# Kernel tuning notes

Measured on AMD Instinct MI355X. Metric: run time of the kernel, lower is better.

## Reference

```python
import jax, jax.numpy as jnp
import numpy as np

B = 256          # number of trees
DEPTH = 8        # complete binary tree depth -> 9 levels
M = 2 ** (DEPTH + 1) - 1   # 511 nodes per tree
N = B * M        # 130816 total nodes
X_SIZE = 128
H_SIZE = 128


def _build_forest():
    j = np.arange(M)
    parent_local = np.maximum((j - 1) // 2, 0)
    lvl = np.array([int(x + 1).bit_length() - 1 for x in j], dtype=np.int32)
    off = (np.arange(B) * M).astype(np.int32)
    parent = (parent_local[None, :] + off[:, None]).reshape(-1).astype(np.int32)
    level = np.tile(lvl, B)
    tree_id = np.repeat(np.arange(B, dtype=np.int32), M)
    isleaf = (level == DEPTH)
    jj = j[1:]
    edge_src = (jj[None, :] + off[:, None]).reshape(-1).astype(np.int32)   # child
    edge_dst = parent[edge_src]                                            # parent
    return parent, level, tree_id, isleaf, edge_src, edge_dst, off


def setup_inputs() -> dict:
    key = jax.random.key(0)
    ks = jax.random.split(key, 12)
    _, level, tree_id, isleaf, edge_src, edge_dst, root_ids = _build_forest()
    sx = 1.0 / np.sqrt(X_SIZE)
    sh = 1.0 / np.sqrt(H_SIZE)
    sxh = 1.0 / np.sqrt(X_SIZE + H_SIZE)
    inp = {
        "X": jax.random.normal(ks[0], (N, X_SIZE), dtype=jnp.float32),
        "h0": jnp.zeros((N, H_SIZE), jnp.float32),
        "c0": jnp.zeros((N, H_SIZE), jnp.float32),
        # bottom-up cell params
        "W_iou_bu": jax.random.normal(ks[1], (3 * H_SIZE, X_SIZE), dtype=jnp.float32) * sx,
        "U_iou_bu": jax.random.normal(ks[2], (3 * H_SIZE, H_SIZE), dtype=jnp.float32) * sh,
        "b_iou_bu": jnp.zeros((1, 3 * H_SIZE), jnp.float32),
        "Uf_bu": jax.random.normal(ks[3], (H_SIZE, H_SIZE), dtype=jnp.float32) * sh,
        "bf_bu": jax.random.normal(ks[4], (H_SIZE,), dtype=jnp.float32) * sh,
        # top-down cell params (x_size = X_SIZE + H_SIZE)
        "W_iou_td": jax.random.normal(ks[5], (3 * H_SIZE, X_SIZE + H_SIZE), dtype=jnp.float32) * sxh,
        "U_iou_td": jax.random.normal(ks[6], (3 * H_SIZE, H_SIZE), dtype=jnp.float32) * sh,
        "b_iou_td": jnp.zeros((1, 3 * H_SIZE), jnp.float32),
        "Uf_td": jax.random.normal(ks[7], (H_SIZE, H_SIZE), dtype=jnp.float32) * sh,
        "bf_td": jax.random.normal(ks[8], (H_SIZE,), dtype=jnp.float32) * sh,
        # graph structure
        "edge_src": jnp.asarray(edge_src),
        "edge_dst": jnp.asarray(edge_dst),
        "level": jnp.asarray(level),
        "tree_id": jnp.asarray(tree_id),
        "isleaf": jnp.asarray(isleaf),
        "root_ids": jnp.asarray(root_ids),
    }
    return inp


def _propagate(X_in, W_iou, U_iou, b_iou, Uf, bf, src, dst, level, no_in, h0, c0, order):
    """Level-synchronous ChildSum TreeLSTM propagation (== dgl.prop_nodes_topo)."""
    n = X_in.shape[0]
    WX = X_in @ W_iou.T                                   # [N, 3H]
    h, c = h0, c0
    for t in order:
        h_src = h[src]                                    # [E, H] gather child/parent states
        c_src = c[src]
        h_tild = jax.ops.segment_sum(h_src, dst, num_segments=n)
        f = jax.nn.sigmoid(h_src @ Uf.T + bf)             # per-edge forget gate
        c_red = jax.ops.segment_sum(f * c_src, dst, num_segments=n)
        iou = WX + h_tild @ U_iou.T + b_iou
        i, o, u = jnp.split(iou, 3, axis=1)
        c_base = jnp.where(no_in[:, None], c0, c_red)     # frontier nodes with no in-edges keep init c
        c_new = jax.nn.sigmoid(i) * jnp.tanh(u) + c_base
        h_new = jax.nn.sigmoid(o) * jnp.tanh(c_new)
        m = (level == t)[:, None]                          # only commit current topological level
        h = jnp.where(m, h_new, h)
        c = jnp.where(m, c_new, c)
    return h


def reference(X, h0, c0, W_iou_bu, U_iou_bu, b_iou_bu, Uf_bu, bf_bu,
              W_iou_td, U_iou_td, b_iou_td, Uf_td, bf_td,
              edge_src, edge_dst, level, tree_id, isleaf, root_ids):
    # bottom-up: messages flow child -> parent, leaves first
    h_bu = _propagate(X, W_iou_bu, U_iou_bu, b_iou_bu, Uf_bu, bf_bu,
                      edge_src, edge_dst, level, isleaf, h0, c0,
                      order=range(DEPTH, -1, -1))
    # top-down: reversed edges, root first
    X_td = jnp.concatenate([X, h_bu], axis=1)
    h_td = _propagate(X_td, W_iou_td, U_iou_td, b_iou_td, Uf_td, bf_td,
                      edge_dst, edge_src, level, level == 0, h0, c0,
                      order=range(0, DEPTH + 1))
    root_h_bottom_up = h_bu[root_ids]                     # [B, H]
    leaf = isleaf.astype(h_td.dtype)
    sums = jax.ops.segment_sum(h_td * leaf[:, None], tree_id, num_segments=root_ids.shape[0])
    cnt = jax.ops.segment_sum(leaf, tree_id, num_segments=root_ids.shape[0])
    leaves_h_top_down = sums / cnt[:, None]               # per-tree mean over leaves
    return jnp.concatenate([root_h_bottom_up, leaves_h_top_down], axis=1)
```

## Files before the change

kernel.cpp:

```cpp
#include <hip/hip_runtime.h>
#include <cmath>

#define NTREE 256
#define MPT 511
#define NNODE (NTREE * MPT)
#define HS 128

typedef __bf16 bf16x8 __attribute__((ext_vector_type(8)));
typedef float  f32x4  __attribute__((ext_vector_type(4)));

__device__ __forceinline__ float sigf(float x) {
  float e = __builtin_amdgcn_exp2f(x * -1.44269504f);
  return __builtin_amdgcn_rcpf(1.0f + e);
}
__device__ __forceinline__ float tanh_fast(float x) {
  float e = __builtin_amdgcn_exp2f(x * -2.88539008f);
  return __builtin_amdgcn_rcpf(1.0f + e) * 2.0f - 1.0f;
}
__device__ __forceinline__ f32x4 mm(bf16x8 a, bf16x8 b, f32x4 c) {
  return __builtin_amdgcn_mfma_f32_16x16x32_bf16(a, b, c, 0, 0, 0);
}
__device__ __forceinline__ int swz(int row, int rb, int kb) { return row * rb + (kb ^ ((row & 7) << 4)); }
__device__ __forceinline__ void st8(char* s, int row, int rb, int chunk, bf16x8 v) {
  *reinterpret_cast<bf16x8*>(s + swz(row, rb, chunk * 16)) = v;
}
__device__ __forceinline__ bf16x8 ld8(const char* s, int row, int rb, int kb) {
  return *reinterpret_cast<const bf16x8*>(s + swz(row, rb, kb));
}
__device__ __forceinline__ bf16x8 g8(const __bf16* p) { return *reinterpret_cast<const bf16x8*>(p); }
__device__ __forceinline__ bf16x8 gx8(const float* p) {
  float4 v0 = reinterpret_cast<const float4*>(p)[0];
  float4 v1 = reinterpret_cast<const float4*>(p)[1];
  bf16x8 o;
  o[0] = (__bf16)v0.x; o[1] = (__bf16)v0.y; o[2] = (__bf16)v0.z; o[3] = (__bf16)v0.w;
  o[4] = (__bf16)v1.x; o[5] = (__bf16)v1.y; o[6] = (__bf16)v1.z; o[7] = (__bf16)v1.w;
  return o;
}
__device__ __forceinline__ void stbf(char* s, int row, int rb, int kbyte, float v) {
  *reinterpret_cast<__bf16*>(s + row * rb + (kbyte ^ ((row & 7) << 4))) = (__bf16)v;
}

__global__ void __launch_bounds__(512, 1)
bu_bottom(const float* __restrict__ Xf,
          const __bf16* __restrict__ W, const float* __restrict__ bp,
          const __bf16* __restrict__ Uf, const float* __restrict__ bf_,
          __bf16* __restrict__ h_bu, float* __restrict__ cws)
{
  __shared__ __align__(16) char sX8[64 * 256];
  __shared__ __align__(16) char sX7[32 * 256];
  __shared__ __align__(16) char sT [32 * 256];
  __shared__ float sCr[32][128];

  const int tid = threadIdx.x, w = tid >> 6, l = tid & 63, lr = l & 15, lk = l >> 4;
  const int ch = w * 16 + lr;
  const int vb = blockIdx.x * 32;
  const int b  = vb >> 7;
  const int j7 = 127 + (vb & 127);
  const size_t g7  = (size_t)b * MPT + j7;
  const size_t gLf = (size_t)b * MPT + 2 * j7 + 1;
  const size_t gp6 = (size_t)b * MPT + ((j7 - 1) >> 1);

  bf16x8 Wb[8][3], Uff[4];
#pragma unroll
  for (int ks = 0; ks < 8; ++ks)
#pragma unroll
    for (int g2 = 0; g2 < 3; ++g2)
      Wb[ks][g2] = g8(W + (size_t)(g2 * 128 + ch) * 256 + ks * 32 + lk * 8);
#pragma unroll
  for (int ks = 0; ks < 4; ++ks) Uff[ks] = g8(Uf + (size_t)ch * HS + ks * 32 + lk * 8);

#pragma unroll
  for (int it = 0; it < 2; ++it) {
    int idx = tid + it * 512, n = idx >> 4, e = idx & 15;
    st8(sX8, n, 256, e, gx8(Xf + (gLf + n) * HS + e * 8));
  }
  { int n = tid >> 4, e = tid & 15;
    st8(sX7, n, 256, e, gx8(Xf + (g7 + n) * HS + e * 8)); }

  const float bia = bp[ch], boa = bp[ch + 128], bua = bp[ch + 256], bfa = bf_[ch];
  __syncthreads();

  f32x4 acc[3][4];
#pragma unroll
  for (int g2 = 0; g2 < 3; ++g2)
#pragma unroll
    for (int mf = 0; mf < 4; ++mf) acc[g2][mf] = 0.0f;

#pragma unroll
  for (int ks = 0; ks < 4; ++ks) {
    const int kb = ks * 64 + lk * 16;
    bf16x8 A0 = ld8(sX8, lr,      256, kb);
    bf16x8 A1 = ld8(sX8, 16 + lr, 256, kb);
    bf16x8 A2 = ld8(sX8, 32 + lr, 256, kb);
    bf16x8 A3 = ld8(sX8, 48 + lr, 256, kb);
#pragma unroll
    for (int g2 = 0; g2 < 3; ++g2) {
      acc[g2][0] = mm(A0, Wb[ks][g2], acc[g2][0]);
      acc[g2][1] = mm(A1, Wb[ks][g2], acc[g2][1]);
      acc[g2][2] = mm(A2, Wb[ks][g2], acc[g2][2]);
      acc[g2][3] = mm(A3, Wb[ks][g2], acc[g2][3]);
    }
  }
  float cnv[4][4], hnv[4][4];
#pragma unroll
  for (int mf = 0; mf < 4; ++mf)
#pragma unroll
    for (int j = 0; j < 4; ++j) {
      const int nrow = 16 * mf + lk * 4 + j;
      float cn = sigf(acc[0][mf][j] + bia) * tanh_fast(acc[2][mf][j] + bua);
      float hn = sigf(acc[1][mf][j] + boa) * tanh_fast(cn);
      cnv[mf][j] = cn; hnv[mf][j] = hn;
      h_bu[(gLf + nrow) * HS + ch] = (__bf16)hn;
    }
  __syncthreads();
#pragma unroll
  for (int mf = 0; mf < 4; ++mf)
#pragma unroll
    for (int j = 0; j < 4; ++j)
      stbf(sX8, 16 * mf + lk * 4 + j, 256, 2 * ch, hnv[mf][j]);
  __syncthreads();
  {
    f32x4 fa[4];
#pragma unroll
    for (int mf = 0; mf < 4; ++mf) fa[mf] = 0.0f;
#pragma unroll
    for (int ks = 0; ks < 4; ++ks) {
      const int kb = ks * 64 + lk * 16;
      fa[0] = mm(ld8(sX8, lr,      256, kb), Uff[ks], fa[0]);
      fa[1] = mm(ld8(sX8, 16 + lr, 256, kb), Uff[ks], fa[1]);
      fa[2] = mm(ld8(sX8, 32 + lr, 256, kb), Uff[ks], fa[2]);
      fa[3] = mm(ld8(sX8, 48 + lr, 256, kb), Uff[ks], fa[3]);
    }
#pragma unroll
    for (int mf = 0; mf < 4; ++mf)
#pragma unroll
      for (int p = 0; p < 2; ++p) {
        const int er = 16 * mf + lk * 4 + 2 * p;
        const int pr = er >> 1;
        float f0 = sigf(fa[mf][2 * p]     + bfa) * cnv[mf][2 * p];
        float f1 = sigf(fa[mf][2 * p + 1] + bfa) * cnv[mf][2 * p + 1];
        sCr[pr][ch] = f0 + f1;
        stbf(sT, pr, 256, 2 * ch, hnv[mf][2 * p] + hnv[mf][2 * p + 1]);
      }
  }
  __syncthreads();

  f32x4 ac2[3][2];
#pragma unroll
  for (int g2 = 0; g2 < 3; ++g2) { ac2[g2][0] = 0.0f; ac2[g2][1] = 0.0f; }
#pragma unroll
  for (int ks = 0; ks < 8; ++ks) {
    const int kb = (ks & 3) * 64 + lk * 16;
    bf16x8 A0 = (ks < 4) ? ld8(sX7, lr,      256, kb) : ld8(sT, lr,      256, kb);
    bf16x8 A1 = (ks < 4) ? ld8(sX7, 16 + lr, 256, kb) : ld8(sT, 16 + lr, 256, kb);
#pragma unroll
    for (int g2 = 0; g2 < 3; ++g2) {
      ac2[g2][0] = mm(A0, Wb[ks][g2], ac2[g2][0]);
      ac2[g2][1] = mm(A1, Wb[ks][g2], ac2[g2][1]);
    }
  }
  float cn2[2][4], hn2[2][4];
#pragma unroll
  for (int mf = 0; mf < 2; ++mf)
#pragma unroll
    for (int j = 0; j < 4; ++j) {
      const int nr = 16 * mf + lk * 4 + j;
      float cn = sigf(ac2[0][mf][j] + bia) * tanh_fast(ac2[2][mf][j] + bua) + sCr[nr][ch];
      float hn = sigf(ac2[1][mf][j] + boa) * tanh_fast(cn);
      cn2[mf][j] = cn; hn2[mf][j] = hn;
      h_bu[(g7 + nr) * HS + ch] = (__bf16)hn;
    }
  __syncthreads();
#pragma unroll
  for (int mf = 0; mf < 2; ++mf)
#pragma unroll
    for (int j = 0; j < 4; ++j)
      stbf(sX7, 16 * mf + lk * 4 + j, 256, 2 * ch, hn2[mf][j]);
  __syncthreads();
  {
    f32x4 fb[2]; fb[0] = 0.0f; fb[1] = 0.0f;
#pragma unroll
    for (int ks = 0; ks < 4; ++ks) {
      const int kb = ks * 64 + lk * 16;
      fb[0] = mm(ld8(sX7, lr,      256, kb), Uff[ks], fb[0]);
      fb[1] = mm(ld8(sX7, 16 + lr, 256, kb), Uff[ks], fb[1]);
    }
#pragma unroll
    for (int mf = 0; mf < 2; ++mf)
#pragma unroll
      for (int p = 0; p < 2; ++p) {
        const int er = 16 * mf + lk * 4 + 2 * p;
        const size_t gp = gp6 + (er >> 1);
        float f0 = sigf(fb[mf][2 * p]     + bfa) * cn2[mf][2 * p];
        float f1 = sigf(fb[mf][2 * p + 1] + bfa) * cn2[mf][2 * p + 1];
        cws[gp * HS + ch] = f0 + f1;
        h_bu[gp * HS + ch] = (__bf16)(hn2[mf][2 * p] + hn2[mf][2 * p + 1]);
      }
  }
}

__global__ void __launch_bounds__(512, 1)
td_bottom(const float* __restrict__ Xf,
          const __bf16* __restrict__ W, const float* __restrict__ bp,
          const __bf16* __restrict__ Uf, const float* __restrict__ bf_,
          const __bf16* __restrict__ h_bu, const __bf16* __restrict__ h_td,
          const float* __restrict__ cws, float* __restrict__ part)
{
  __shared__ __align__(16) char sA7[32 * 768];
  __shared__ __align__(16) char sXH[64 * 512];
  __shared__ __align__(16) char sTd[32 * 256];
  __shared__ float sFc[32][128];

  const int tid = threadIdx.x, w = tid >> 6, l = tid & 63, lr = l & 15, lk = l >> 4;
  const int ch = w * 16 + lr;
  const int vb = blockIdx.x * 32;
  const int b  = vb >> 7;
  const int j7 = 127 + (vb & 127);
  const size_t g7  = (size_t)b * MPT + j7;
  const size_t gLf = (size_t)b * MPT + 2 * j7 + 1;
  const size_t gp6 = (size_t)b * MPT + ((j7 - 1) >> 1);

  bf16x8 Wt[12][3], Uff[4];
#pragma unroll
  for (int ks = 0; ks < 12; ++ks)
#pragma unroll
    for (int g2 = 0; g2 < 3; ++g2)
      Wt[ks][g2] = g8(W + (size_t)(g2 * 128 + ch) * 384 + ks * 32 + lk * 8);
#pragma unroll
  for (int ks = 0; ks < 4; ++ks) Uff[ks] = g8(Uf + (size_t)ch * HS + ks * 32 + lk * 8);

  { int n = tid >> 4, e = tid & 15;
    st8(sA7, n, 768, e,      gx8(Xf   + (g7 + n) * HS + e * 8));
    st8(sA7, n, 768, 16 + e, g8(h_bu + (g7 + n) * HS + e * 8));
    st8(sA7, n, 768, 32 + e, g8(h_td + (gp6 + (n >> 1)) * HS + e * 8)); }
#pragma unroll
  for (int it = 0; it < 2; ++it) {
    int idx = tid + it * 512, n = idx >> 4, e = idx & 15;
    st8(sXH, n, 512, e,      gx8(Xf   + (gLf + n) * HS + e * 8));
    st8(sXH, n, 512, 16 + e, g8(h_bu + (gLf + n) * HS + e * 8));
  }
  float cb[2][4];
#pragma unroll
  for (int mf = 0; mf < 2; ++mf)
#pragma unroll
    for (int j = 0; j < 4; ++j) {
      const int nr = 16 * mf + lk * 4 + j;
      cb[mf][j] = cws[(gp6 + (nr >> 1)) * HS + ch];
    }
  const float bia = bp[ch], boa = bp[ch + 128], bua = bp[ch + 256], bfa = bf_[ch];
  __syncthreads();

  f32x4 ac[3][2];
#pragma unroll
  for (int g2 = 0; g2 < 3; ++g2) { ac[g2][0] = 0.0f; ac[g2][1] = 0.0f; }
#pragma unroll
  for (int ks = 0; ks < 12; ++ks) {
    const int kb = ks * 64 + lk * 16;
    bf16x8 A0 = ld8(sA7, lr,      768, kb);
    bf16x8 A1 = ld8(sA7, 16 + lr, 768, kb);
#pragma unroll
    for (int g2 = 0; g2 < 3; ++g2) {
      ac[g2][0] = mm(A0, Wt[ks][g2], ac[g2][0]);
      ac[g2][1] = mm(A1, Wt[ks][g2], ac[g2][1]);
    }
  }
  float cn7[2][4];
#pragma unroll
  for (int mf = 0; mf < 2; ++mf)
#pragma unroll
    for (int j = 0; j < 4; ++j) {
      const int nr = 16 * mf + lk * 4 + j;
      float cn = sigf(ac[0][mf][j] + bia) * tanh_fast(ac[2][mf][j] + bua) + cb[mf][j];
      float hn = sigf(ac[1][mf][j] + boa) * tanh_fast(cn);
      cn7[mf][j] = cn;
      stbf(sTd, nr, 256, 2 * ch, hn);
    }
  __syncthreads();
  {
    f32x4 fa[2]; fa[0] = 0.0f; fa[1] = 0.0f;
#pragma unroll
    for (int ks = 0; ks < 4; ++ks) {
      const int kb = ks * 64 + lk * 16;
      fa[0] = mm(ld8(sTd, lr,      256, kb), Uff[ks], fa[0]);
      fa[1] = mm(ld8(sTd, 16 + lr, 256, kb), Uff[ks], fa[1]);
    }
#pragma unroll
    for (int mf = 0; mf < 2; ++mf)
#pragma unroll
      for (int j = 0; j < 4; ++j) {
        const int nr = 16 * mf + lk * 4 + j;
        sFc[nr][ch] = sigf(fa[mf][j] + bfa) * cn7[mf][j];
      }
  }
  __syncthreads();

  f32x4 a8[3][4];
#pragma unroll
  for (int g2 = 0; g2 < 3; ++g2)
#pragma unroll
    for (int mf = 0; mf < 4; ++mf) a8[g2][mf] = 0.0f;
#pragma unroll
  for (int ks = 0; ks < 12; ++ks) {
    bf16x8 A0, A1, A2, A3;
    if (ks < 8) {
      const int kb = ks * 64 + lk * 16;
      A0 = ld8(sXH, lr,      512, kb);
      A1 = ld8(sXH, 16 + lr, 512, kb);
      A2 = ld8(sXH, 32 + lr, 512, kb);
      A3 = ld8(sXH, 48 + lr, 512, kb);
    } else {
      const int kb = (ks - 8) * 64 + lk * 16;
      A0 = ld8(sTd, (lr >> 1),      256, kb);
      A1 = ld8(sTd, 8 + (lr >> 1),  256, kb);
      A2 = ld8(sTd, 16 + (lr >> 1), 256, kb);
      A3 = ld8(sTd, 24 + (lr >> 1), 256, kb);
    }
#pragma unroll
    for (int g2 = 0; g2 < 3; ++g2) {
      a8[g2][0] = mm(A0, Wt[ks][g2], a8[g2][0]);
      a8[g2][1] = mm(A1, Wt[ks][g2], a8[g2][1]);
      a8[g2][2] = mm(A2, Wt[ks][g2], a8[g2][2]);
      a8[g2][3] = mm(A3, Wt[ks][g2], a8[g2][3]);
    }
  }
  float psum = 0.0f;
#pragma unroll
  for (int mf = 0; mf < 4; ++mf)
#pragma unroll
    for (int j = 0; j < 4; ++j) {
      const int nrow = 16 * mf + lk * 4 + j;
      float cbase = sFc[nrow >> 1][ch];
      float cn = sigf(a8[0][mf][j] + bia) * tanh_fast(a8[2][mf][j] + bua) + cbase;
      float hn = sigf(a8[1][mf][j] + boa) * tanh_fast(cn);
      psum += hn;
    }
  float s = psum;
  s += __shfl_xor(s, 16);
  s += __shfl_xor(s, 32);
  if (lk == 0) part[(size_t)blockIdx.x * 128 + ch] = s;
}

template <int MODE>
__global__ void __launch_bounds__(256, 2)
level_big(int t,
          const float*  __restrict__ Xf,
          const __bf16* __restrict__ W,
          const float*  __restrict__ bp,
          const __bf16* __restrict__ Uf,
          const float*  __restrict__ bf_,
          __bf16* __restrict__ h_bu,
          __bf16* __restrict__ h_td,
          float*  __restrict__ cws)
{
  constexpr int KA = (MODE == 1) ? 256 : 384;
  constexpr int KS = KA / 32;
  constexpr int BK = (MODE == 3) ? 384 : 256;
  constexpr int RB = KA * 2;
  constexpr int HB = (MODE == 1) ? 256 : 512;

  __shared__ __align__(16) char sA[64 * RB];
  __shared__ int sG[64], sP[64];

  const int tid = threadIdx.x;
  const int w = tid >> 6, l = tid & 63, lr = l & 15, lk = l >> 4;

  if (tid < 64) {
    int v = blockIdx.x * 64 + tid;
    int b = v >> t;
    int j = (1 << t) - 1 + (v & ((1 << t) - 1));
    sG[tid] = b * MPT + j;
    sP[tid] = b * MPT + ((j - 1) >> 1);
  }
  __syncthreads();

#pragma unroll
  for (int it = 0; it < 4; ++it) {
    int idx = tid + it * 256, n = idx >> 4, e = idx & 15;
    st8(sA, n, RB, e, gx8(Xf + (size_t)sG[n] * HS + e * 8));
  }
#pragma unroll
  for (int it = 0; it < 4; ++it) {
    int idx = tid + it * 256, n = idx >> 4, e = idx & 15;
    st8(sA, n, RB, 16 + e, g8(h_bu + (size_t)sG[n] * HS + e * 8));
  }
  if constexpr (MODE == 3) {
#pragma unroll
    for (int it = 0; it < 4; ++it) {
      int idx = tid + it * 256, n = idx >> 4, e = idx & 15;
      st8(sA, n, RB, 32 + e, g8(h_td + (size_t)sP[n] * HS + e * 8));
    }
  }
  __syncthreads();

  float cb[2][4][4];
  float bia[2], boa[2], bua[2], bfa[2];
#pragma unroll
  for (int nf = 0; nf < 2; ++nf) {
    const int ch = w * 32 + nf * 16 + lr;
    bia[nf] = bp[ch]; boa[nf] = bp[ch + 128]; bua[nf] = bp[ch + 256];
    bfa[nf] = bf_[ch];
#pragma unroll
    for (int mf = 0; mf < 4; ++mf)
#pragma unroll
      for (int j = 0; j < 4; ++j) {
        const int nrow = 16 * mf + lk * 4 + j;
        const int src = (MODE == 1) ? sG[nrow] : sP[nrow];
        cb[nf][mf][j] = cws[(size_t)src * HS + ch];
      }
  }

  f32x4 acc[6][4];
#pragma unroll
  for (int p = 0; p < 6; ++p)
#pragma unroll
    for (int mf = 0; mf < 4; ++mf) acc[p][mf] = 0.0f;

  bf16x8 A0[4], A1[4], Bb[3][6];
  auto ldA = [&](int ks, bf16x8* Ad) {
#pragma unroll
    for (int mf = 0; mf < 4; ++mf) Ad[mf] = ld8(sA, mf * 16 + lr, RB, ks * 64 + lk * 16);
  };
  auto ldB = [&](int ks, int s) {
#pragma unroll
    for (int g2 = 0; g2 < 3; ++g2)
#pragma unroll
      for (int nf = 0; nf < 2; ++nf)
        Bb[s][g2 * 2 + nf] = g8(W + (size_t)(g2 * 128 + w * 32 + nf * 16 + lr) * BK + ks * 32 + lk * 8);
  };

  ldB(0, 0); ldA(0, A0); ldB(1, 1);
#pragma unroll
  for (int ks = 0; ks < KS; ++ks) {
    bf16x8* Ac = (ks & 1) ? A1 : A0;
    bf16x8* An = (ks & 1) ? A0 : A1;
    if (ks + 1 < KS) ldA(ks + 1, An);
    if (ks + 2 < KS) ldB(ks + 2, (ks + 2) % 3);
#pragma unroll
    for (int p = 0; p < 6; ++p)
#pragma unroll
      for (int mf = 0; mf < 4; ++mf) acc[p][mf] = mm(Ac[mf], Bb[ks % 3][p], acc[p][mf]);
  }

  bf16x8 Uff[8];
#pragma unroll
  for (int ks = 0; ks < 4; ++ks)
#pragma unroll
    for (int nf = 0; nf < 2; ++nf)
      Uff[ks * 2 + nf] = g8(Uf + (size_t)(w * 32 + nf * 16 + lr) * HS + ks * 32 + lk * 8);

  __bf16* hp = (MODE == 3) ? h_td : h_bu;
  float cnv[2][4][4], hnv[2][4][4];
#pragma unroll
  for (int nf = 0; nf < 2; ++nf) {
    const int ch = w * 32 + nf * 16 + lr;
#pragma unroll
    for (int mf = 0; mf < 4; ++mf)
#pragma unroll
      for (int j = 0; j < 4; ++j) {
        const int nrow = 16 * mf + lk * 4 + j;
        float cn = sigf(acc[nf][mf][j] + bia[nf]) * tanh_fast(acc[4 + nf][mf][j] + bua[nf]) + cb[nf][mf][j];
        float hn = sigf(acc[2 + nf][mf][j] + boa[nf]) * tanh_fast(cn);
        hp[(size_t)sG[nrow] * HS + ch] = (__bf16)hn;
        cnv[nf][mf][j] = cn; hnv[nf][mf][j] = hn;
      }
  }

  __syncthreads();
#pragma unroll
  for (int nf = 0; nf < 2; ++nf) {
    const int ch = w * 32 + nf * 16 + lr;
#pragma unroll
    for (int mf = 0; mf < 4; ++mf)
#pragma unroll
      for (int j = 0; j < 4; ++j)
        stbf(sA, 16 * mf + lk * 4 + j, RB, HB + 2 * ch, hnv[nf][mf][j]);
  }
  __syncthreads();
  f32x4 fa[4][2];
#pragma unroll
  for (int mf = 0; mf < 4; ++mf) { fa[mf][0] = 0.0f; fa[mf][1] = 0.0f; }
#pragma unroll
  for (int ks = 0; ks < 4; ++ks) {
    bf16x8 a0 = ld8(sA, lr,      RB, HB + ks * 64 + lk * 16);
    bf16x8 a1 = ld8(sA, 16 + lr, RB, HB + ks * 64 + lk * 16);
    bf16x8 a2 = ld8(sA, 32 + lr, RB, HB + ks * 64 + lk * 16);
    bf16x8 a3 = ld8(sA, 48 + lr, RB, HB + ks * 64 + lk * 16);
#pragma unroll
    for (int nf = 0; nf < 2; ++nf) {
      fa[0][nf] = mm(a0, Uff[ks * 2 + nf], fa[0][nf]);
      fa[1][nf] = mm(a1, Uff[ks * 2 + nf], fa[1][nf]);
      fa[2][nf] = mm(a2, Uff[ks * 2 + nf], fa[2][nf]);
      fa[3][nf] = mm(a3, Uff[ks * 2 + nf], fa[3][nf]);
    }
  }
#pragma unroll
  for (int nf = 0; nf < 2; ++nf) {
    const int ch = w * 32 + nf * 16 + lr;
    if constexpr (MODE == 3) {
#pragma unroll
      for (int mf = 0; mf < 4; ++mf)
#pragma unroll
        for (int j = 0; j < 4; ++j) {
          const int nrow = 16 * mf + lk * 4 + j;
          cws[(size_t)sG[nrow] * HS + ch] = sigf(fa[mf][nf][j] + bfa[nf]) * cnv[nf][mf][j];
        }
    } else {
#pragma unroll
      for (int mf = 0; mf < 4; ++mf)
#pragma unroll
        for (int p = 0; p < 2; ++p) {
          const int er = 16 * mf + lk * 4 + 2 * p;
          float f0 = sigf(fa[mf][nf][2 * p]     + bfa[nf]) * cnv[nf][mf][2 * p];
          float f1 = sigf(fa[mf][nf][2 * p + 1] + bfa[nf]) * cnv[nf][mf][2 * p + 1];
          const int gp = sP[er];
          cws[(size_t)gp * HS + ch] = f0 + f1;
          h_bu[(size_t)gp * HS + ch] = (__bf16)(hnv[nf][mf][2 * p] + hnv[nf][mf][2 * p + 1]);
        }
    }
  }
}

__global__ void __launch_bounds__(512, 2)
small_both(const float* __restrict__ Xf,
           const __bf16* __restrict__ Wbu, const float* __restrict__ bbu,
           const __bf16* __restrict__ Ufb, const float* __restrict__ bfb,
           const __bf16* __restrict__ Wtd, const float* __restrict__ btd,
           const __bf16* __restrict__ Uft, const float* __restrict__ bft,
           __bf16* __restrict__ h_bu, __bf16* __restrict__ h_td,
           float* __restrict__ cws)
{
  __shared__ __align__(16) char sX[31 * 256];
  __shared__ __align__(16) char sH[31 * 256];
  __shared__ __align__(16) char sT[16 * 256];
  __shared__ __align__(16) char sTd[15 * 256];
  __shared__ float sCr[16][128];
  __shared__ float sFc[16][128];

  const int tid = threadIdx.x, w = tid >> 6, l = tid & 63, lr = l & 15, lk = l >> 4;
  const int ch = w * 16 + lr;
  const size_t base = (size_t)blockIdx.x * MPT * HS;

  for (int idx = tid; idx < 31 * 16; idx += 512) {
    int n = idx >> 4, e = idx & 15;
    st8(sX, n, 256, e, gx8(Xf + base + (size_t)n * HS + e * 8));
  }
  if (tid < 256) { int n = tid >> 4, e = tid & 15;
    st8(sT, n, 256, e, g8(h_bu + base + (size_t)(15 + n) * HS + e * 8)); }
  { int n = tid >> 5, e = tid & 31;
    reinterpret_cast<float4*>(&sCr[n][0])[e] =
        reinterpret_cast<const float4*>(cws + base + (size_t)(15 + n) * HS)[e]; }
  for (int idx = tid; idx < 15 * 16; idx += 512)
    *reinterpret_cast<float4*>(sTd + idx * 16) = float4{0.f, 0.f, 0.f, 0.f};

  {
    const float bia = bbu[ch], boa = bbu[ch + 128], bua = bbu[ch + 256], bfa = bfb[ch];
    bf16x8 Wb[8][3], Uff[4];
#pragma unroll
    for (int ks = 0; ks < 8; ++ks)
#pragma unroll
      for (int g2 = 0; g2 < 3; ++g2)
        Wb[ks][g2] = g8(Wbu + (size_t)(g2 * 128 + ch) * 256 + ks * 32 + lk * 8);
#pragma unroll
    for (int ks = 0; ks < 4; ++ks)
      Uff[ks] = g8(Ufb + (size_t)ch * HS + ks * 32 + lk * 8);
    __syncthreads();

    for (int t = 4; t >= 0; --t) {
      const int cnt = 1 << t, j0 = cnt - 1;
      f32x4 acc0 = 0.0f, acc1 = 0.0f, acc2 = 0.0f;
      bf16x8 Aa[3];
      auto ldA = [&](int ks, int s) {
        const int kb = (ks & 3) * 64 + lk * 16;
        Aa[s] = (ks < 4) ? ld8(sX, j0 + lr, 256, kb) : ld8(sT, lr, 256, kb);
      };
      ldA(0, 0); ldA(1, 1);
#pragma unroll
      for (int ks = 0; ks < 8; ++ks) {
        if (ks + 2 < 8) ldA(ks + 2, (ks + 2) % 3);
        acc0 = mm(Aa[ks % 3], Wb[ks][0], acc0);
        acc1 = mm(Aa[ks % 3], Wb[ks][1], acc1);
        acc2 = mm(Aa[ks % 3], Wb[ks][2], acc2);
      }
      float cnv[4], hnv[4];
#pragma unroll
      for (int j = 0; j < 4; ++j) {
        const int r = lk * 4 + j;
        float cn = sigf(acc0[j] + bia) * tanh_fast(acc2[j] + bua) + sCr[r][ch];
        float hn = sigf(acc1[j] + boa) * tanh_fast(cn);
        cnv[j] = cn; hnv[j] = hn;
        if (r < cnt) stbf(sH, j0 + r, 256, 2 * ch, hn);
      }
      if (t == 0 && lk == 0) h_bu[base + ch] = (__bf16)hnv[0];
      __syncthreads();
      if (t > 0) {
        f32x4 fa = 0.0f;
#pragma unroll
        for (int ks = 0; ks < 4; ++ks)
          fa = mm(ld8(sH, j0 + lr, 256, ks * 64 + lk * 16), Uff[ks], fa);
#pragma unroll
        for (int p = 0; p < 2; ++p) {
          const int pr = lk * 2 + p;
          if (pr < (cnt >> 1)) {
            float f0 = sigf(fa[2 * p]     + bfa) * cnv[2 * p];
            float f1 = sigf(fa[2 * p + 1] + bfa) * cnv[2 * p + 1];
            sCr[pr][ch] = f0 + f1;
            stbf(sT, pr, 256, 2 * ch, hnv[2 * p] + hnv[2 * p + 1]);
          }
        }
      }
      __syncthreads();
    }
  }

  {
    const float bia = btd[ch], boa = btd[ch + 128], bua = btd[ch + 256], bfa = bft[ch];
    bf16x8 Wt[12][3], Uff[4];
#pragma unroll
    for (int ks = 0; ks < 12; ++ks)
#pragma unroll
      for (int g2 = 0; g2 < 3; ++g2)
        Wt[ks][g2] = g8(Wtd + (size_t)(g2 * 128 + ch) * 384 + ks * 32 + lk * 8);
#pragma unroll
    for (int ks = 0; ks < 4; ++ks)
      Uff[ks] = g8(Uft + (size_t)ch * HS + ks * 32 + lk * 8);

    for (int t = 0; t <= 4; ++t) {
      const int cnt = 1 << t, j0 = cnt - 1;
      f32x4 acc0 = 0.0f, acc1 = 0.0f, acc2 = 0.0f;
      bf16x8 Aa[3];
      auto ldA = [&](int ks, int s) {
        const int kb = (ks & 3) * 64 + lk * 16;
        if (ks < 4)      Aa[s] = ld8(sX, j0 + lr, 256, kb);
        else if (ks < 8) Aa[s] = ld8(sH, j0 + lr, 256, kb);
        else { int pr = (j0 + lr - 1) >> 1; pr = pr < 0 ? 0 : pr;
               Aa[s] = ld8(sTd, pr, 256, kb); }
      };
      ldA(0, 0); ldA(1, 1);
#pragma unroll
      for (int ks = 0; ks < 12; ++ks) {
        if (ks + 2 < 12) ldA(ks + 2, (ks + 2) % 3);
        acc0 = mm(Aa[ks % 3], Wt[ks][0], acc0);
        acc1 = mm(Aa[ks % 3], Wt[ks][1], acc1);
        acc2 = mm(Aa[ks % 3], Wt[ks][2], acc2);
      }
      float cnv[4], hnv[4];
#pragma unroll
      for (int j = 0; j < 4; ++j) {
        const int r = lk * 4 + j;
        float cbv = (t == 0) ? 0.0f : sFc[r >> 1][ch];
        float cn = sigf(acc0[j] + bia) * tanh_fast(acc2[j] + bua) + cbv;
        float hn = sigf(acc1[j] + boa) * tanh_fast(cn);
        cnv[j] = cn; hnv[j] = hn;
        stbf(sT, r, 256, 2 * ch, hn);
        if (r < cnt && j0 + r < 15) stbf(sTd, j0 + r, 256, 2 * ch, hn);
        if (t == 4) h_td[base + (size_t)(15 + r) * HS + ch] = (__bf16)hn;
      }
      __syncthreads();
      f32x4 fa = 0.0f;
#pragma unroll
      for (int ks = 0; ks < 4; ++ks)
        fa = mm(ld8(sT, lr, 256, ks * 64 + lk * 16), Uff[ks], fa);
#pragma unroll
      for (int j = 0; j < 4; ++j) {
        const int r = lk * 4 + j;
        float fcv = sigf(fa[j] + bfa) * cnv[j];
        if (r < cnt) {
          if (t < 4) sFc[r][ch] = fcv;
          else       cws[base + (size_t)(15 + r) * HS + ch] = fcv;
        }
      }
      __syncthreads();
    }
  }
}

__global__ void __launch_bounds__(256)
prep(const float* __restrict__ Wbu, const float* __restrict__ Ubu,
     const float* __restrict__ Wtd, const float* __restrict__ Utd,
     const float* __restrict__ Ufb, const float* __restrict__ Uft,
     __bf16* wbu, __bf16* wtd, __bf16* ufb, __bf16* uft)
{
  int i = blockIdx.x * 256 + threadIdx.x;
  if (i < 98304) {
    int r = i >> 8, c = i & 255;
    wbu[i] = (__bf16)(c < 128 ? Wbu[r * 128 + c] : Ubu[r * 128 + c - 128]);
  } else if (i < 245760) {
    int k = i - 98304; int r = k / 384, c = k - r * 384;
    wtd[k] = (__bf16)(c < 256 ? Wtd[r * 256 + c] : Utd[r * 128 + (c - 256)]);
  } else if (i < 262144) {
    int k = i - 245760; ufb[k] = (__bf16)Ufb[k];
  } else {
    int k = i - 262144; uft[k] = (__bf16)Uft[k];
  }
}

__global__ void __launch_bounds__(128)
finalize_kernel(const __bf16* __restrict__ h_bu, const float* __restrict__ part,
                float* __restrict__ out)
{
  int b = blockIdx.x, ch = threadIdx.x;
  out[(size_t)b * 256 + ch] = (float)h_bu[((size_t)b * MPT) * HS + ch];
  const float* pp = part + (size_t)b * 512 + ch;
  out[(size_t)b * 256 + 128 + ch] = (pp[0] + pp[128] + pp[256] + pp[384]) * (1.0f / 256.0f);
}

extern "C" void kernel_launch(void* const* d_in, const int* in_sizes, int n_in,
                              void* d_out, int out_size, void* d_ws, size_t ws_size,
                              hipStream_t stream) {
  const float* X     = (const float*)d_in[0];
  const float* W_bu  = (const float*)d_in[3];
  const float* U_bu  = (const float*)d_in[4];
  const float* b_bu  = (const float*)d_in[5];
  const float* Uf_bu = (const float*)d_in[6];
  const float* bf_bu = (const float*)d_in[7];
  const float* W_td  = (const float*)d_in[8];
  const float* U_td  = (const float*)d_in[9];
  const float* b_td  = (const float*)d_in[10];
  const float* Uf_td = (const float*)d_in[11];
  const float* bf_td = (const float*)d_in[12];

  char* p = (char*)d_ws;
  __bf16* wbu  = (__bf16*)p; p += (size_t)384 * 256 * 2;
  __bf16* wtd  = (__bf16*)p; p += (size_t)384 * 384 * 2;
  __bf16* ufb  = (__bf16*)p; p += (size_t)128 * 128 * 2;
  __bf16* uft  = (__bf16*)p; p += (size_t)128 * 128 * 2;
  __bf16* h_bu = (__bf16*)p; p += (size_t)NNODE * HS * 2;
  __bf16* h_td = (__bf16*)p; p += (size_t)NNODE * HS * 2;
  float*  cws  = (float*)p;  p += (size_t)NNODE * HS * 4;
  float*  part = (float*)p;

  prep<<<1088, 256, 0, stream>>>(W_bu, U_bu, W_td, U_td, Uf_bu, Uf_td, wbu, wtd, ufb, uft);

  bu_bottom<<<1024, 512, 0, stream>>>(X, wbu, b_bu, ufb, bf_bu, h_bu, cws);
  level_big<1><<<256, 256, 0, stream>>>(6, X, wbu, b_bu, ufb, bf_bu, h_bu, h_td, cws);
  level_big<1><<<128, 256, 0, stream>>>(5, X, wbu, b_bu, ufb, bf_bu, h_bu, h_td, cws);

  small_both<<<256, 512, 0, stream>>>(X, wbu, b_bu, ufb, bf_bu,
                                      wtd, b_td, uft, bf_td, h_bu, h_td, cws);

  level_big<3><<<128, 256, 0, stream>>>(5, X, wtd, b_td, uft, bf_td, h_bu, h_td, cws);
  level_big<3><<<256, 256, 0, stream>>>(6, X, wtd, b_td, uft, bf_td, h_bu, h_td, cws);
  td_bottom<<<1024, 512, 0, stream>>>(X, wtd, b_td, uft, bf_td, h_bu, h_td, cws, part);

  finalize_kernel<<<256, 128, 0, stream>>>(h_bu, part, (float*)d_out);
}
```

Measured before the change: 237.2 us.

## Double per-block node tile in bottom-level BU/TD kernels to amortize weight loads

bu_bottom and td_bottom now handle 64 level-7 nodes (128 leaves) per block instead of 32, halving the grid to 512 blocks. Each block loads the full register-resident weight fragments once, so the total weight traffic and setup per node is halved. td_bottom also stages the parent h_td rows once in a separate compact buffer instead of duplicating them per child row. The cost is doubled LDS use and larger accumulator arrays, which raise register pressure and risk spills, and the grid now gives about two blocks per CU.

Measured after the change: 291.0 us. +22.7%, slower.

```diff
diff --git a/kernel.cpp b/kernel.cpp
--- a/kernel.cpp
+++ b/kernel.cpp
@@ -46,14 +46,14 @@
           const __bf16* __restrict__ Uf, const float* __restrict__ bf_,
           __bf16* __restrict__ h_bu, float* __restrict__ cws)
 {
-  __shared__ __align__(16) char sX8[64 * 256];
-  __shared__ __align__(16) char sX7[32 * 256];
-  __shared__ __align__(16) char sT [32 * 256];
-  __shared__ float sCr[32][128];
+  __shared__ __align__(16) char sX8[128 * 256];
+  __shared__ __align__(16) char sX7[64 * 256];
+  __shared__ __align__(16) char sT [64 * 256];
+  __shared__ float sCr[64][128];
 
   const int tid = threadIdx.x, w = tid >> 6, l = tid & 63, lr = l & 15, lk = l >> 4;
   const int ch = w * 16 + lr;
-  const int vb = blockIdx.x * 32;
+  const int vb = blockIdx.x * 64;
   const int b  = vb >> 7;
   const int j7 = 127 + (vb & 127);
   const size_t g7  = (size_t)b * MPT + j7;
@@ -70,131 +70,135 @@
   for (int ks = 0; ks < 4; ++ks) Uff[ks] = g8(Uf + (size_t)ch * HS + ks * 32 + lk * 8);
 
 #pragma unroll
+  for (int it = 0; it < 4; ++it) {
+    int idx = tid + it * 512, n = idx >> 4, e = idx & 15;
+    st8(sX8, n, 256, e, gx8(Xf + (gLf + n) * HS + e * 8));
+  }
+#pragma unroll
   for (int it = 0; it < 2; ++it) {
     int idx = tid + it * 512, n = idx >> 4, e = idx & 15;
-    st8(sX8, n, 256, e, gx8(Xf + (gLf + n) * HS + e * 8));
-  }
-  { int n = tid >> 4, e = tid & 15;
-    st8(sX7, n, 256, e, gx8(Xf + (g7 + n) * HS + e * 8)); }
+    st8(sX7, n, 256, e, gx8(Xf + (g7 + n) * HS + e * 8));
+  }
 
   const float bia = bp[ch], boa = bp[ch + 128], bua = bp[ch + 256], bfa = bf_[ch];
   __syncthreads();
 
-  f32x4 acc[3][4];
+  f32x4 acc[3][8];
 #pragma unroll
   for (int g2 = 0; g2 < 3; ++g2)
 #pragma unroll
-    for (int mf = 0; mf < 4; ++mf) acc[g2][mf] = 0.0f;
+    for (int q = 0; q < 8; ++q) acc[g2][q] = 0.0f;
 
 #pragma unroll
   for (int ks = 0; ks < 4; ++ks) {
     const int kb = ks * 64 + lk * 16;
-    bf16x8 A0 = ld8(sX8, lr,      256, kb);
-    bf16x8 A1 = ld8(sX8, 16 + lr, 256, kb);
-    bf16x8 A2 = ld8(sX8, 32 + lr, 256, kb);
-    bf16x8 A3 = ld8(sX8, 48 + lr, 256, kb);
-#pragma unroll
-    for (int g2 = 0; g2 < 3; ++g2) {
-      acc[g2][0] = mm(A0, Wb[ks][g2], acc[g2][0]);
-      acc[g2][1] = mm(A1, Wb[ks][g2], acc[g2][1]);
-      acc[g2][2] = mm(A2, Wb[ks][g2], acc[g2][2]);
-      acc[g2][3] = mm(A3, Wb[ks][g2], acc[g2][3]);
-    }
-  }
-  float cnv[4][4], hnv[4][4];
-#pragma unroll
-  for (int mf = 0; mf < 4; ++mf)
+    bf16x8 Aq[8];
+#pragma unroll
+    for (int q = 0; q < 8; ++q) Aq[q] = ld8(sX8, 16 * q + lr, 256, kb);
+#pragma unroll
+    for (int g2 = 0; g2 < 3; ++g2)
+#pragma unroll
+      for (int q = 0; q < 8; ++q) acc[g2][q] = mm(Aq[q], Wb[ks][g2], acc[g2][q]);
+  }
+  float cnv[8][4], hnv[8][4];
+#pragma unroll
+  for (int q = 0; q < 8; ++q)
 #pragma unroll
     for (int j = 0; j < 4; ++j) {
-      const int nrow = 16 * mf + lk * 4 + j;
-      float cn = sigf(acc[0][mf][j] + bia) * tanh_fast(acc[2][mf][j] + bua);
-      float hn = sigf(acc[1][mf][j] + boa) * tanh_fast(cn);
-      cnv[mf][j] = cn; hnv[mf][j] = hn;
+      const int nrow = 16 * q + lk * 4 + j;
+      float cn = sigf(acc[0][q][j] + bia) * tanh_fast(acc[2][q][j] + bua);
+      float hn = sigf(acc[1][q][j] + boa) * tanh_fast(cn);
+      cnv[q][j] = cn; hnv[q][j] = hn;
       h_bu[(gLf + nrow) * HS + ch] = (__bf16)hn;
     }
   __syncthreads();
 #pragma unroll
-  for (int mf = 0; mf < 4; ++mf)
+  for (int q = 0; q < 8; ++q)
 #pragma unroll
     for (int j = 0; j < 4; ++j)
-      stbf(sX8, 16 * mf + lk * 4 + j, 256, 2 * ch, hnv[mf][j]);
+      stbf(sX8, 16 * q + lk * 4 + j, 256, 2 * ch, hnv[q][j]);
   __syncthreads();
   {
-    f32x4 fa[4];
-#pragma unroll
-    for (int mf = 0; mf < 4; ++mf) fa[mf] = 0.0f;
+    f32x4 fa[8];
+#pragma unroll
+    for (int q = 0; q < 8; ++q) fa[q] = 0.0f;
 #pragma unroll
     for (int ks = 0; ks < 4; ++ks) {
       const int kb = ks * 64 + lk * 16;
-      fa[0] = mm(ld8(sX8, lr,      256, kb), Uff[ks], fa[0]);
-      fa[1] = mm(ld8(sX8, 16 + lr, 256, kb), Uff[ks], fa[1]);
-      fa[2] = mm(ld8(sX8, 32 + lr, 256, kb), Uff[ks], fa[2]);
-      fa[3] = mm(ld8(sX8, 48 + lr, 256, kb), Uff[ks], fa[3]);
-    }
-#pragma unroll
-    for (int mf = 0; mf < 4; ++mf)
+#pragma unroll
+      for (int q = 0; q < 8; ++q)
+        fa[q] = mm(ld8(sX8, 16 * q + lr, 256, kb), Uff[ks], fa[q]);
+    }
+#pragma unroll
+    for (int q = 0; q < 8; ++q)
 #pragma unroll
       for (int p = 0; p < 2; ++p) {
-        const int er = 16 * mf + lk * 4 + 2 * p;
+        const int er = 16 * q + lk * 4 + 2 * p;
         const int pr = er >> 1;
-        float f0 = sigf(fa[mf][2 * p]     + bfa) * cnv[mf][2 * p];
-        float f1 = sigf(fa[mf][2 * p + 1] + bfa) * cnv[mf][2 * p + 1];
+        float f0 = sigf(fa[q][2 * p]     + bfa) * cnv[q][2 * p];
+        float f1 = sigf(fa[q][2 * p + 1] + bfa) * cnv[q][2 * p + 1];
         sCr[pr][ch] = f0 + f1;
-        stbf(sT, pr, 256, 2 * ch, hnv[mf][2 * p] + hnv[mf][2 * p + 1]);
-      }
-  }
-  __syncthreads();
-
-  f32x4 ac2[3][2];
-#pragma unroll
-  for (int g2 = 0; g2 < 3; ++g2) { ac2[g2][0] = 0.0f; ac2[g2][1] = 0.0f; }
+        stbf(sT, pr, 256, 2 * ch, hnv[q][2 * p] + hnv[q][2 * p + 1]);
+      }
+  }
+  __syncthreads();
+
+  f32x4 ac2[3][4];
+#pragma unroll
+  for (int g2 = 0; g2 < 3; ++g2)
+#pragma unroll
+    for (int q = 0; q < 4; ++q) ac2[g2][q] = 0.0f;
 #pragma unroll
   for (int ks = 0; ks < 8; ++ks) {
     const int kb = (ks & 3) * 64 + lk * 16;
-    bf16x8 A0 = (ks < 4) ? ld8(sX7, lr,      256, kb) : ld8(sT, lr,      256, kb);
-    bf16x8 A1 = (ks < 4) ? ld8(sX7, 16 + lr, 256, kb) : ld8(sT, 16 + lr, 256, kb);
-#pragma unroll
-    for (int g2 = 0; g2 < 3; ++g2) {
-      ac2[g2][0] = mm(A0, Wb[ks][g2], ac2[g2][0]);
-      ac2[g2][1] = mm(A1, Wb[ks][g2], ac2[g2][1]);
-    }
-  }
-  float cn2[2][4], hn2[2][4];
-#pragma unroll
-  for (int mf = 0; mf < 2; ++mf)
+    bf16x8 Aq[4];
+#pragma unroll
+    for (int q = 0; q < 4; ++q)
+      Aq[q] = (ks < 4) ? ld8(sX7, 16 * q + lr, 256, kb) : ld8(sT, 16 * q + lr, 256, kb);
+#pragma unroll
+    for (int g2 = 0; g2 < 3; ++g2)
+#pragma unroll
+      for (int q = 0; q < 4; ++q) ac2[g2][q] = mm(Aq[q], Wb[ks][g2], ac2[g2][q]);
+  }
+  float cn2[4][4], hn2[4][4];
+#pragma unroll
+  for (int q = 0; q < 4; ++q)
 #pragma unroll
     for (int j = 0; j < 4; ++j) {
-      const int nr = 16 * mf + lk * 4 + j;
-      float cn = sigf(ac2[0][mf][j] + bia) * tanh_fast(ac2[2][mf][j] + bua) + sCr[nr][ch];
-      float hn = sigf(ac2[1][mf][j] + boa) * tanh_fast(cn);
-      cn2[mf][j] = cn; hn2[mf][j] = hn;
+      const int nr = 16 * q + lk * 4 + j;
+      float cn = sigf(ac2[0][q][j] + bia) * tanh_fast(ac2[2][q][j] + bua) + sCr[nr][ch];
+      float hn = sigf(ac2[1][q][j] + boa) * tanh_fast(cn);
+      cn2[q][j] = cn; hn2[q][j] = hn;
       h_bu[(g7 + nr) * HS + ch] = (__bf16)hn;
     }
   __syncthreads();
 #pragma unroll
-  for (int mf = 0; mf < 2; ++mf)
+  for (int q = 0; q < 4; ++q)
 #pragma unroll
     for (int j = 0; j < 4; ++j)
-      stbf(sX7, 16 * mf + lk * 4 + j, 256, 2 * ch, hn2[mf][j]);
+      stbf(sX7, 16 * q + lk * 4 + j, 256, 2 * ch, hn2[q][j]);
   __syncthreads();
   {
-    f32x4 fb[2]; fb[0] = 0.0f; fb[1] = 0.0f;
+    f32x4 fb[4];
+#pragma unroll
+    for (int q = 0; q < 4; ++q) fb[q] = 0.0f;
 #pragma unroll
     for (int ks = 0; ks < 4; ++ks) {
       const int kb = ks * 64 + lk * 16;
-      fb[0] = mm(ld8(sX7, lr,      256, kb), Uff[ks], fb[0]);
-      fb[1] = mm(ld8(sX7, 16 + lr, 256, kb), Uff[ks], fb[1]);
-    }
-#pragma unroll
-    for (int mf = 0; mf < 2; ++mf)
+#pragma unroll
+      for (int q = 0; q < 4; ++q)
+        fb[q] = mm(ld8(sX7, 16 * q + lr, 256, kb), Uff[ks], fb[q]);
+    }
+#pragma unroll
+    for (int q = 0; q < 4; ++q)
 #pragma unroll
       for (int p = 0; p < 2; ++p) {
-        const int er = 16 * mf + lk * 4 + 2 * p;
+        const int er = 16 * q + lk * 4 + 2 * p;
         const size_t gp = gp6 + (er >> 1);
-        float f0 = sigf(fb[mf][2 * p]     + bfa) * cn2[mf][2 * p];
-        float f1 = sigf(fb[mf][2 * p + 1] + bfa) * cn2[mf][2 * p + 1];
+        float f0 = sigf(fb[q][2 * p]     + bfa) * cn2[q][2 * p];
+        float f1 = sigf(fb[q][2 * p + 1] + bfa) * cn2[q][2 * p + 1];
         cws[gp * HS + ch] = f0 + f1;
-        h_bu[gp * HS + ch] = (__bf16)(hn2[mf][2 * p] + hn2[mf][2 * p + 1]);
+        h_bu[gp * HS + ch] = (__bf16)(hn2[q][2 * p] + hn2[q][2 * p + 1]);
       }
   }
 }
@@ -206,14 +210,15 @@
           const __bf16* __restrict__ h_bu, const __bf16* __restrict__ h_td,
           const float* __restrict__ cws, float* __restrict__ part)
 {
-  __shared__ __align__(16) char sA7[32 * 768];
-  __shared__ __align__(16) char sXH[64 * 512];
-  __shared__ __align__(16) char sTd[32 * 256];
-  __shared__ float sFc[32][128];
+  __shared__ __align__(16) char sA7[64 * 512];
+  __shared__ __align__(16) char sPar[32 * 256];
+  __shared__ __align__(16) char sXH[128 * 512];
+  __shared__ __align__(16) char sTd[64 * 256];
+  __shared__ float sFc[64][128];
 
   const int tid = threadIdx.x, w = tid >> 6, l = tid & 63, lr = l & 15, lk = l >> 4;
   const int ch = w * 16 + lr;
-  const int vb = blockIdx.x * 32;
+  const int vb = blockIdx.x * 64;
   const int b  = vb >> 7;
   const int j7 = 127 + (vb & 127);
   const size_t g7  = (size_t)b * MPT + j7;
@@ -229,109 +234,118 @@
 #pragma unroll
   for (int ks = 0; ks < 4; ++ks) Uff[ks] = g8(Uf + (size_t)ch * HS + ks * 32 + lk * 8);
 
+#pragma unroll
+  for (int it = 0; it < 2; ++it) {
+    int idx = tid + it * 512, n = idx >> 4, e = idx & 15;
+    st8(sA7, n, 512, e,      gx8(Xf   + (g7 + n) * HS + e * 8));
+    st8(sA7, n, 512, 16 + e, g8(h_bu + (g7 + n) * HS + e * 8));
+  }
   { int n = tid >> 4, e = tid & 15;
-    st8(sA7, n, 768, e,      gx8(Xf   + (g7 + n) * HS + e * 8));
-    st8(sA7, n, 768, 16 + e, g8(h_bu + (g7 + n) * HS + e * 8));
-    st8(sA7, n, 768, 32 + e, g8(h_td + (gp6 + (n >> 1)) * HS + e * 8)); }
-#pragma unroll
-  for (int it = 0; it < 2; ++it) {
+    if (tid < 512) st8(sPar, n & 31, 256, e,
+                       g8(h_td + (gp6 + (n & 31)) * HS + e * 8)); }
+#pragma unroll
+  for (int it = 0; it < 4; ++it) {
     int idx = tid + it * 512, n = idx >> 4, e = idx & 15;
     st8(sXH, n, 512, e,      gx8(Xf   + (gLf + n) * HS + e * 8));
     st8(sXH, n, 512, 16 + e, g8(h_bu + (gLf + n) * HS + e * 8));
   }
-  float cb[2][4];
-#pragma unroll
-  for (int mf = 0; mf < 2; ++mf)
+  float cb[4][4];
+#pragma unroll
+  for (int q = 0; q < 4; ++q)
 #pragma unroll
     for (int j = 0; j < 4; ++j) {
-      const int nr = 16 * mf + lk * 4 + j;
-      cb[mf][j] = cws[(gp6 + (nr >> 1)) * HS + ch];
+      const int nr = 16 * q + lk * 4 + j;
+      cb[q][j] = cws[(gp6 + (nr >> 1)) * HS + ch];
     }
   const float bia = bp[ch], boa = bp[ch + 128], bua = bp[ch + 256], bfa = bf_[ch];
   __syncthreads();
 
-  f32x4 ac[3][2];
-#pragma unroll
-  for (int g2 = 0; g2 < 3; ++g2) { ac[g2][0] = 0.0f; ac[g2][1] = 0.0f; }
+  f32x4 ac[3][4];
+#pragma unroll
+  for (int g2 = 0; g2 < 3; ++g2)
+#pragma unroll
+    for (int q = 0; q < 4; ++q) ac[g2][q] = 0.0f;
 #pragma unroll
   for (int ks = 0; ks < 12; ++ks) {
-    const int kb = ks * 64 + lk * 16;
-    bf16x8 A0 = ld8(sA7, lr,      768, kb);
-    bf16x8 A1 = ld8(sA7, 16 + lr, 768, kb);
-#pragma unroll
-    for (int g2 = 0; g2 < 3; ++g2) {
-      ac[g2][0] = mm(A0, Wt[ks][g2], ac[g2][0]);
-      ac[g2][1] = mm(A1, Wt[ks][g2], ac[g2][1]);
-    }
-  }
-  float cn7[2][4];
-#pragma unroll
-  for (int mf = 0; mf < 2; ++mf)
+    bf16x8 Aq[4];
+    if (ks < 8) {
+      const int kb = ks * 64 + lk * 16;
+#pragma unroll
+      for (int q = 0; q < 4; ++q) Aq[q] = ld8(sA7, 16 * q + lr, 512, kb);
+    } else {
+      const int kb = (ks - 8) * 64 + lk * 16;
+#pragma unroll
+      for (int q = 0; q < 4; ++q) Aq[q] = ld8(sPar, 8 * q + (lr >> 1), 256, kb);
+    }
+#pragma unroll
+    for (int g2 = 0; g2 < 3; ++g2)
+#pragma unroll
+      for (int q = 0; q < 4; ++q) ac[g2][q] = mm(Aq[q], Wt[ks][g2], ac[g2][q]);
+  }
+  float cn7[4][4];
+#pragma unroll
+  for (int q = 0; q < 4; ++q)
 #pragma unroll
     for (int j = 0; j < 4; ++j) {
-      const int nr = 16 * mf + lk * 4 + j;
-      float cn = sigf(ac[0][mf][j] + bia) * tanh_fast(ac[2][mf][j] + bua) + cb[mf][j];
-      float hn = sigf(ac[1][mf][j] + boa) * tanh_fast(cn);
-      cn7[mf][j] = cn;
+      const int nr = 16 * q + lk * 4 + j;
+      float cn = sigf(ac[0][q][j] + bia) * tanh_fast(ac[2][q][j] + bua) + cb[q][j];
+      float hn = sigf(ac[1][q][j] + boa) * tanh_fast(cn);
+      cn7[q][j] = cn;
       stbf(sTd, nr, 256, 2 * ch, hn);
     }
   __syncthreads();
   {
-    f32x4 fa[2]; fa[0] = 0.0f; fa[1] = 0.0f;
+    f32x4 fa[4];
+#pragma unroll
+    for (int q = 0; q < 4; ++q) fa[q] = 0.0f;
 #pragma unroll
     for (int ks = 0; ks < 4; ++ks) {
       const int kb = ks * 64 + lk * 16;
-      fa[0] = mm(ld8(sTd, lr,      256, kb), Uff[ks], fa[0]);
-      fa[1] = mm(ld8(sTd, 16 + lr, 256, kb), Uff[ks], fa[1]);
-    }
-#pragma unroll
-    for (int mf = 0; mf < 2; ++mf)
+#pragma unroll
+      for (int q = 0; q < 4; ++q)
+        fa[q] = mm(ld8(sTd, 16 * q + lr, 256, kb), Uff[ks], fa[q]);
+    }
+#pragma unroll
+    for (int q = 0; q < 4; ++q)
 #pragma unroll
       for (int j = 0; j < 4; ++j) {
-        const int nr = 16 * mf + lk * 4 + j;
-        sFc[nr][ch] = sigf(fa[mf][j] + bfa) * cn7[mf][j];
-      }
-  }
-  __syncthreads();
-
-  f32x4 a8[3][4];
+        const int nr = 16 * q + lk * 4 + j;
+        sFc[nr][ch] = sigf(fa[q][j] + bfa) * cn7[q][j];
+      }
+  }
+  __syncthreads();
+
+  f32x4 a8[3][8];
 #pragma unroll
   for (int g2 = 0; g2 < 3; ++g2)
 #pragma unroll
-    for (int mf = 0; mf < 4; ++mf) a8[g2][mf] = 0.0f;
+    for (int q = 0; q < 8; ++q) a8[g2][q] = 0.0f;
 #pragma unroll
   for (int ks = 0; ks < 12; ++ks) {
-    bf16x8 A0, A1, A2, A3;
+    bf16x8 Aq[8];
     if (ks < 8) {
       const int kb = ks * 64 + lk * 16;
-      A0 = ld8(sXH, lr,      512, kb);
-      A1 = ld8(sXH, 16 + lr, 512, kb);
-      A2 = ld8(sXH, 32 + lr, 512, kb);
-      A3 = ld8(sXH, 48 + lr, 512, kb);
+#pragma unroll
+      for (int q = 0; q < 8; ++q) Aq[q] = ld8(sXH, 16 * q + lr, 512, kb);
     } else {
       const int kb = (ks - 8) * 64 + lk * 16;
-      A0 = ld8(sTd, (lr >> 1),      256, kb);
-      A1 = ld8(sTd, 8 + (lr >> 1),  256, kb);
-      A2 = ld8(sTd, 16 + (lr >> 1), 256, kb);
-      A3 = ld8(sTd, 24 + (lr >> 1), 256, kb);
-    }
-#pragma unroll
-    for (int g2 = 0; g2 < 3; ++g2) {
-      a8[g2][0] = mm(A0, Wt[ks][g2], a8[g2][0]);
-      a8[g2][1] = mm(A1, Wt[ks][g2], a8[g2][1]);
-      a8[g2][2] = mm(A2, Wt[ks][g2], a8[g2][2]);
-      a8[g2][3] = mm(A3, Wt[ks][g2], a8[g2][3]);
-    }
+#pragma unroll
+      for (int q = 0; q < 8; ++q) Aq[q] = ld8(sTd, 8 * q + (lr >> 1), 256, kb);
+    }
+#pragma unroll
+    for (int g2 = 0; g2 < 3; ++g2)
+#pragma unroll
+      for (int q = 0; q < 8; ++q) a8[g2][q] = mm(Aq[q], Wt[ks][g2], a8[g2][q]);
   }
   float psum = 0.0f;
 #pragma unroll
-  for (int mf = 0; mf < 4; ++mf)
+  for (int q = 0; q < 8; ++q)
 #pragma unroll
     for (int j = 0; j < 4; ++j) {
-      const int nrow = 16 * mf + lk * 4 + j;
+      const int nrow = 16 * q + lk * 4 + j;
       float cbase = sFc[nrow >> 1][ch];
-      float cn = sigf(a8[0][mf][j] + bia) * tanh_fast(a8[2][mf][j] + bua) + cbase;
-      float hn = sigf(a8[1][mf][j] + boa) * tanh_fast(cn);
+      float cn = sigf(a8[0][q][j] + bia) * tanh_fast(a8[2][q][j] + bua) + cbase;
+      float hn = sigf(a8[1][q][j] + boa) * tanh_fast(cn);
       psum += hn;
     }
   float s = psum;
@@ -700,8 +714,8 @@
 {
   int b = blockIdx.x, ch = threadIdx.x;
   out[(size_t)b * 256 + ch] = (float)h_bu[((size_t)b * MPT) * HS + ch];
-  const float* pp = part + (size_t)b * 512 + ch;
-  out[(size_t)b * 256 + 128 + ch] = (pp[0] + pp[128] + pp[256] + pp[384]) * (1.0f / 256.0f);
+  const float* pp = part + (size_t)b * 256 + ch;
+  out[(size_t)b * 256 + 128 + ch] = (pp[0] + pp[128]) * (1.0f / 256.0f);
 }
 
 extern "C" void kernel_launch(void* const* d_in, const int* in_sizes, int n_in,
@@ -731,7 +745,7 @@
 
   prep<<<1088, 256, 0, stream>>>(W_bu, U_bu, W_td, U_td, Uf_bu, Uf_td, wbu, wtd, ufb, uft);
 
-  bu_bottom<<<1024, 512, 0, stream>>>(X, wbu, b_bu, ufb, bf_bu, h_bu, cws);
+  bu_bottom<<<512, 512, 0, stream>>>(X, wbu, b_bu, ufb, bf_bu, h_bu, cws);
   level_big<1><<<256, 256, 0, stream>>>(6, X, wbu, b_bu, ufb, bf_bu, h_bu, h_td, cws);
   level_big<1><<<128, 256, 0, stream>>>(5, X, wbu, b_bu, ufb, bf_bu, h_bu, h_td, cws);
 
@@ -740,7 +754,7 @@
 
   level_big<3><<<128, 256, 0, stream>>>(5, X, wtd, b_td, uft, bf_td, h_bu, h_td, cws);
   level_big<3><<<256, 256, 0, stream>>>(6, X, wtd, b_td, uft, bf_td, h_bu, h_td, cws);
-  td_bottom<<<1024, 512, 0, stream>>>(X, wtd, b_td, uft, bf_td, h_bu, h_td, cws, part);
+  td_bottom<<<512, 512, 0, stream>>>(X, wtd, b_td, uft, bf_td, h_bu, h_td, cws, part);
 
   finalize_kernel<<<256, 128, 0, stream>>>(h_bu, part, (float*)d_out);
 }
```
